# Optimization experiments

Measured on AMD Instinct MI355X. Metric: run time of the kernel, lower is better.

Reference implementation:

```python
import jax, jax.numpy as jnp
import numpy as np

D_MODEL = 768
N_LAYER = 4
VOCAB = 10000
N_MELS = 80
D_STATE = 16
D_CONV = 4
DT_RANK = 48          # ceil(768/16)
D_INNER = 1536        # expand * d_model
B_SZ, L_SEQ = 2, 1024


def rmsnorm(x, w, eps=1e-5):
    return x * jax.lax.rsqrt(jnp.mean(x * x, axis=-1, keepdims=True) + eps) * w


def causal_depthwise_conv(x, w, b):
    # x: (b, l, d_inner); w: (d_inner, 1, d_conv); torch Conv1d with padding=d_conv-1, truncated to l
    xc = jax.lax.conv_general_dilated(
        jnp.transpose(x, (0, 2, 1)), w, window_strides=(1,),
        padding=[(D_CONV - 1, 0)], dimension_numbers=('NCH', 'OIH', 'NCH'),
        feature_group_count=D_INNER)
    xc = xc + b[None, :, None]
    return jnp.transpose(xc, (0, 2, 1))


def selective_scan(u, dt, A, B, C, D):
    # u, dt: (b,l,d_in); A: (d_in,n); B,C: (b,l,n); D: (d_in,)
    dA = jnp.einsum('bld,dn->bldn', dt, A)
    dB_u = jnp.einsum('bld,bld,bln->bldn', dt, u, B)
    dA = jnp.clip(dA, -20, None)
    # shift dA by one step (exclusive cumulative decay), cumsum mode
    dA_shift = jnp.pad(dA[:, 1:], ((0, 0), (1, 0), (0, 0), (0, 0)))
    dA_cumsum = jnp.exp(jnp.cumsum(dA_shift, axis=1))
    x = jnp.cumsum(dB_u / (dA_cumsum + 1e-12), axis=1) * dA_cumsum
    y = jnp.einsum('bldn,bln->bld', x, C)
    return y + u * D


def mamba_block(x, rms_w, in_w, cw, cb, xp_w, dt_w, dt_b, A_log, Dp, out_w):
    h = rmsnorm(x, rms_w)
    xz = h @ in_w                       # (b,l,2*d_inner)
    xi, res = jnp.split(xz, 2, axis=-1)
    xi = jax.nn.silu(causal_depthwise_conv(xi, cw, cb))
    A = -jnp.exp(A_log.astype(jnp.float32))
    x_dbl = xi @ xp_w                   # (b,l,dt_rank+2n)
    delta = x_dbl[..., :DT_RANK]
    Bm = x_dbl[..., DT_RANK:DT_RANK + D_STATE]
    Cm = x_dbl[..., DT_RANK + D_STATE:]
    delta = jax.nn.softplus(delta @ dt_w + dt_b)
    y = selective_scan(xi, delta, A, Bm, Cm, Dp.astype(jnp.float32))
    y = y * jax.nn.silu(res)
    return y @ out_w + x


def setup_inputs():
    key = jax.random.key(0)
    ks = jax.random.split(key, 8)
    s = 0.02
    return {
        'input_ids': jax.random.randint(ks[0], (B_SZ, L_SEQ), 0, VOCAB),
        'embedding': jax.random.normal(ks[1], (VOCAB, D_MODEL), jnp.float32) * s,
        'rms_w': jnp.ones((N_LAYER, D_MODEL), jnp.float32),
        'in_proj_w': jax.random.normal(ks[2], (N_LAYER, D_MODEL, 2 * D_INNER), jnp.float32) * s,
        'conv_w': jax.random.normal(ks[3], (N_LAYER, D_INNER, 1, D_CONV), jnp.float32) * 0.1,
        'conv_b': jnp.zeros((N_LAYER, D_INNER), jnp.float32),
        'x_proj_w': jax.random.normal(ks[4], (N_LAYER, D_INNER, DT_RANK + 2 * D_STATE), jnp.float32) * s,
        'dt_proj_w': jax.random.normal(ks[5], (N_LAYER, DT_RANK, D_INNER), jnp.float32) * s,
        'dt_proj_b': jnp.zeros((N_LAYER, D_INNER), jnp.float32),
        'A_log': jnp.broadcast_to(jnp.log(jnp.arange(1, D_STATE + 1, dtype=jnp.float32)), (N_LAYER, D_INNER, D_STATE)) + 0.0,
        'D_param': jnp.ones((N_LAYER, D_INNER), jnp.float32),
        'out_proj_w': jax.random.normal(ks[6], (N_LAYER, D_INNER, D_MODEL), jnp.float32) * s,
        'norm_f_w': jnp.ones((D_MODEL,), jnp.float32),
        'head_w': jax.random.normal(ks[7], (D_MODEL, N_MELS), jnp.float32) * s,
    }


def reference(input_ids, embedding, rms_w, in_proj_w, conv_w, conv_b, x_proj_w,
              dt_proj_w, dt_proj_b, A_log, D_param, out_proj_w, norm_f_w, head_w):
    x = embedding[input_ids]            # (b,l,d)
    for i in range(N_LAYER):
        x = mamba_block(x, rms_w[i], in_proj_w[i], conv_w[i], conv_b[i],
                        x_proj_w[i], dt_proj_w[i], dt_proj_b[i], A_log[i],
                        D_param[i], out_proj_w[i])
    x = rmsnorm(x, norm_f_w)
    return x @ head_w                   # (b,l,n_mels)
```

## Files before the change

kernel.cpp:

```cpp
#include <hip/hip_runtime.h>
#include <hip/hip_bf16.h>
#include <math.h>

#define D_MODEL 768
#define N_LAYER 4
#define D_STATE 16
#define D_CONV  4
#define DT_RANK 48
#define D_INNER 1536
#define B_SZ    2
#define L_SEQ   1024
#define N_MELS  80
#define ROWS    (B_SZ * L_SEQ)

typedef __bf16 bf16x8 __attribute__((ext_vector_type(8)));
typedef float  f32x4  __attribute__((ext_vector_type(4)));

__device__ __forceinline__ float fast_exp2(float x) {
    float r; asm("v_exp_f32 %0, %1" : "=v"(r) : "v"(x)); return r;
}
__device__ __forceinline__ float fast_exp(float x) {
    return fast_exp2(x * 1.44269504f);
}
__device__ __forceinline__ float fast_rcp(float x) {
    float r; asm("v_rcp_f32 %0, %1" : "=v"(r) : "v"(x)); return r;
}
__device__ __forceinline__ float silu_f(float v) {
    return v * fast_rcp(1.0f + fast_exp(-v));
}
__device__ __forceinline__ float softplus_f(float v) {
    return fmaxf(v, 0.0f) + log1pf(expf(-fabsf(v)));
}
__device__ __forceinline__ unsigned short f2bf(float f) {
    unsigned int u = __float_as_uint(f);
    unsigned int r = (u + 0x7FFFu + ((u >> 16) & 1u)) >> 16;
    return (unsigned short)r;
}
__device__ __forceinline__ float bf2f(unsigned short v) {
    return __uint_as_float(((unsigned int)v) << 16);
}

__global__ void embed_kernel(const int* __restrict__ ids,
                             const float* __restrict__ emb,
                             float* __restrict__ x) {
    int i = blockIdx.x * 256 + threadIdx.x;
    if (i >= ROWS * D_MODEL) return;
    int r = i / D_MODEL, c = i - r * D_MODEL;
    x[i] = emb[(size_t)ids[r] * D_MODEL + c];
}

__global__ void rmsnorm_kernel(const float* __restrict__ x,
                               const float* __restrict__ w,
                               unsigned short* __restrict__ hb) {
    int row = blockIdx.x;
    const float* xr = x + (size_t)row * D_MODEL;
    int tid = threadIdx.x;
    float p = 0.f;
    for (int c = tid; c < D_MODEL; c += 256) { float v = xr[c]; p = fmaf(v, v, p); }
    for (int off = 32; off >= 1; off >>= 1) p += __shfl_down(p, off, 64);
    __shared__ float ws[4];
    int lane = tid & 63, wv = tid >> 6;
    if (lane == 0) ws[wv] = p;
    __syncthreads();
    if (tid == 0) ws[0] = ws[0] + ws[1] + ws[2] + ws[3];
    __syncthreads();
    float scale = 1.0f / sqrtf(ws[0] / (float)D_MODEL + 1e-5f);
    for (int c = tid; c < D_MODEL; c += 256)
        hb[(size_t)row * D_MODEL + c] = f2bf(xr[c] * scale * w[c]);
}

__global__ void prep_weights_kernel(const float* __restrict__ in_wi,
                                    const float* __restrict__ out_wi,
                                    const float* __restrict__ xp_wi,
                                    const float* __restrict__ dt_wi,
                                    unsigned short* __restrict__ wt_in,
                                    unsigned short* __restrict__ wt_out,
                                    unsigned short* __restrict__ xpT,
                                    unsigned short* __restrict__ dtwT) {
    __shared__ float t[32][33];
    int bx = blockIdx.x;
    int tid = threadIdx.x;
    if (bx < 3456) {
        const float* src; unsigned short* dst; int R, C, cy, cx;
        if (bx < 2304) {
            src = in_wi; dst = wt_in; R = D_MODEL; C = 2 * D_INNER;
            cy = bx / 96; cx = bx - cy * 96;
        } else {
            int tt = bx - 2304;
            src = out_wi; dst = wt_out; R = D_INNER; C = D_MODEL;
            cy = tt / 24; cx = tt - cy * 24;
        }
        int tx = tid & 31, ty = tid >> 5;
        int r0 = cy * 32, c0 = cx * 32;
#pragma unroll
        for (int i = 0; i < 4; i++)
            t[ty + i * 8][tx] = src[(size_t)(r0 + ty + i * 8) * C + c0 + tx];
        __syncthreads();
#pragma unroll
        for (int i = 0; i < 4; i++)
            dst[(size_t)(c0 + ty + i * 8) * R + r0 + tx] = f2bf(t[tx][ty + i * 8]);
    } else {
        int i = (bx - 3456) * 256 + tid;
        if (i < 80 * D_INNER) {
            int c = i / D_INNER, r = i - c * D_INNER;
            xpT[i] = f2bf(xp_wi[(size_t)r * 80 + c]);
        } else {
            int i2 = i - 80 * D_INNER;
            int c = i2 >> 6, r = i2 & 63;
            dtwT[i2] = (r < DT_RANK) ? f2bf(dt_wi[(size_t)r * D_INNER + c])
                                     : (unsigned short)0;
        }
    }
}

__global__ void transpose_u16_kernel(const unsigned short* __restrict__ src,
                                     unsigned short* __restrict__ dst,
                                     int R, int C) {
    __shared__ unsigned short t[32][34];
    int tx = threadIdx.x & 31, ty = threadIdx.x >> 5;
    int r0 = blockIdx.y * 32, c0 = blockIdx.x * 32;
#pragma unroll
    for (int i = 0; i < 4; i++)
        t[ty + i * 8][tx] = src[(size_t)(r0 + ty + i * 8) * C + c0 + tx];
    __syncthreads();
#pragma unroll
    for (int i = 0; i < 4; i++)
        dst[(size_t)(c0 + ty + i * 8) * R + r0 + tx] = t[tx][ty + i * 8];
}

__global__ void transpose_pad_bf16_kernel(const float* __restrict__ src,
                                          unsigned short* __restrict__ dst,
                                          int R, int C, int Rpad) {
    int i = blockIdx.x * 256 + threadIdx.x;
    if (i >= C * Rpad) return;
    int c = i / Rpad, r = i - c * Rpad;
    dst[i] = (r < R) ? f2bf(src[(size_t)r * C + c]) : (unsigned short)0;
}

__global__ void reduce_cvt_kernel(const float* __restrict__ part,
                                  float* __restrict__ xdbl,
                                  unsigned short* __restrict__ xdblb,
                                  int nsplit) {
    int i = blockIdx.x * 256 + threadIdx.x;
    if (i >= ROWS * 80) return;
    float s = 0.f;
    for (int k = 0; k < nsplit; k++) s += part[(size_t)k * ROWS * 80 + i];
    xdbl[i] = s;
    int r = i / 80, c = i - r * 80;
    if (c < DT_RANK) xdblb[r * 64 + c] = f2bf(s);
    else if (c >= 64) xdblb[r * 64 + c - 16] = 0;
}

__global__ void reduce_split_kernel(const float* __restrict__ part,
                                    float* __restrict__ dst,
                                    int MN, int nsplit) {
    int i = blockIdx.x * 256 + threadIdx.x;
    if (i >= MN) return;
    float s = 0.f;
    for (int k = 0; k < nsplit; k++) s += part[(size_t)k * MN + i];
    dst[i] = s;
}

__global__ __launch_bounds__(256) void mfma_gemm64(
        const unsigned short* __restrict__ A,
        const unsigned short* __restrict__ BT,
        const float* __restrict__ bias, const float* __restrict__ resid,
        float* __restrict__ Cf, unsigned short* __restrict__ Cb,
        int M, int N, int K, int ldc, int act, int bias_mode) {
    __shared__ unsigned short As[64][40];
    __shared__ unsigned short Bs[128][40];
    int tid = threadIdx.x;
    int row0 = blockIdx.y * 64, col0 = blockIdx.x * 128;
    int wave = tid >> 6, lane = tid & 63;
    int wr = (wave >> 1) * 32, wc = (wave & 1) * 64;
    int lm = lane & 15, lq = lane >> 4;
    int ar = tid >> 2, aseg = tid & 3;
    const unsigned short* Ap  = A  + (size_t)(row0 + ar) * K + aseg * 8;
    int br0 = tid >> 2, br1 = (tid + 256) >> 2;
    const unsigned short* Bp0 = BT + (size_t)(col0 + br0) * K + aseg * 8;
    const unsigned short* Bp1 = BT + (size_t)(col0 + br1) * K + aseg * 8;
    f32x4 acc[2][4] = {};
    bf16x8 pa  = *(const bf16x8*)Ap;
    bf16x8 pb0 = *(const bf16x8*)Bp0;
    bf16x8 pb1 = *(const bf16x8*)Bp1;
    *(bf16x8*)&As[ar][aseg * 8]  = pa;
    *(bf16x8*)&Bs[br0][aseg * 8] = pb0;
    *(bf16x8*)&Bs[br1][aseg * 8] = pb1;
    for (int k0 = 0; k0 < K; k0 += 32) {
        __syncthreads();
        bool more = (k0 + 32 < K);
        if (more) {
            pa  = *(const bf16x8*)(Ap  + k0 + 32);
            pb0 = *(const bf16x8*)(Bp0 + k0 + 32);
            pb1 = *(const bf16x8*)(Bp1 + k0 + 32);
        }
        bf16x8 af[2], bfr[4];
#pragma unroll
        for (int i = 0; i < 2; i++) af[i] = *(const bf16x8*)&As[wr + i * 16 + lm][lq * 8];
#pragma unroll
        for (int j = 0; j < 4; j++) bfr[j] = *(const bf16x8*)&Bs[wc + j * 16 + lm][lq * 8];
#pragma unroll
        for (int i = 0; i < 2; i++)
#pragma unroll
            for (int j = 0; j < 4; j++)
                acc[i][j] = __builtin_amdgcn_mfma_f32_16x16x32_bf16(af[i], bfr[j], acc[i][j], 0, 0, 0);
        __syncthreads();
        if (more) {
            *(bf16x8*)&As[ar][aseg * 8]  = pa;
            *(bf16x8*)&Bs[br0][aseg * 8] = pb0;
            *(bf16x8*)&Bs[br1][aseg * 8] = pb1;
        }
    }
#pragma unroll
    for (int i = 0; i < 2; i++) {
#pragma unroll
        for (int ii = 0; ii < 4; ii++) {
            int row = row0 + wr + i * 16 + lq * 4 + ii;
#pragma unroll
            for (int j = 0; j < 4; j++) {
                int col = col0 + wc + j * 16 + lm;
                float v = acc[i][j][ii];
                if (bias) v += bias[bias_mode ? row : col];
                if (act == 1) v = softplus_f(v);
                if (resid) v += resid[(size_t)row * ldc + col];
                if (Cf) Cf[(size_t)row * ldc + col] = v;
                else    Cb[(size_t)row * ldc + col] = f2bf(v);
            }
        }
    }
}

__global__ __launch_bounds__(256) void mfma_gemm32(
        const unsigned short* __restrict__ A,
        const unsigned short* __restrict__ BT,
        const float* __restrict__ bias, const float* __restrict__ resid,
        float* __restrict__ Cf, unsigned short* __restrict__ Cb,
        int M, int N, int K, int ldc, int act, int bias_mode) {
    __shared__ unsigned short As[32][40];
    __shared__ unsigned short Bs[128][40];
    int tid = threadIdx.x;
    int row0 = blockIdx.y * 32, col0 = blockIdx.x * 128;
    int wave = tid >> 6, lane = tid & 63;
    int wc = wave * 32;
    int lm = lane & 15, lq = lane >> 4;
    int ar = tid >> 2, aseg = tid & 3;
    const unsigned short* Ap  = A  + (size_t)(row0 + ar) * K + aseg * 8;
    int br0 = tid >> 2, br1 = (tid + 256) >> 2;
    const unsigned short* Bp0 = BT + (size_t)(col0 + br0) * K + aseg * 8;
    const unsigned short* Bp1 = BT + (size_t)(col0 + br1) * K + aseg * 8;
    bool haveA = (tid < 128);
    f32x4 acc[2][2] = {};
    bf16x8 pa = {};
    if (haveA) pa = *(const bf16x8*)Ap;
    bf16x8 pb0 = *(const bf16x8*)Bp0;
    bf16x8 pb1 = *(const bf16x8*)Bp1;
    if (haveA) *(bf16x8*)&As[ar][aseg * 8] = pa;
    *(bf16x8*)&Bs[br0][aseg * 8] = pb0;
    *(bf16x8*)&Bs[br1][aseg * 8] = pb1;
    for (int k0 = 0; k0 < K; k0 += 32) {
        __syncthreads();
        bool more = (k0 + 32 < K);
        if (more) {
            if (haveA) pa = *(const bf16x8*)(Ap + k0 + 32);
            pb0 = *(const bf16x8*)(Bp0 + k0 + 32);
            pb1 = *(const bf16x8*)(Bp1 + k0 + 32);
        }
        bf16x8 af[2], bfr[2];
#pragma unroll
        for (int i = 0; i < 2; i++) af[i] = *(const bf16x8*)&As[i * 16 + lm][lq * 8];
#pragma unroll
        for (int j = 0; j < 2; j++) bfr[j] = *(const bf16x8*)&Bs[wc + j * 16 + lm][lq * 8];
#pragma unroll
        for (int i = 0; i < 2; i++)
#pragma unroll
            for (int j = 0; j < 2; j++)
                acc[i][j] = __builtin_amdgcn_mfma_f32_16x16x32_bf16(af[i], bfr[j], acc[i][j], 0, 0, 0);
        __syncthreads();
        if (more) {
            if (haveA) *(bf16x8*)&As[ar][aseg * 8] = pa;
            *(bf16x8*)&Bs[br0][aseg * 8] = pb0;
            *(bf16x8*)&Bs[br1][aseg * 8] = pb1;
        }
    }
#pragma unroll
    for (int i = 0; i < 2; i++) {
#pragma unroll
        for (int ii = 0; ii < 4; ii++) {
            int row = row0 + i * 16 + lq * 4 + ii;
#pragma unroll
            for (int j = 0; j < 2; j++) {
                int col = col0 + wc + j * 16 + lm;
                float v = acc[i][j][ii];
                if (bias) v += bias[bias_mode ? row : col];
                if (act == 1) v = softplus_f(v);
                if (resid) v += resid[(size_t)row * ldc + col];
                if (Cf) Cf[(size_t)row * ldc + col] = v;
                else    Cb[(size_t)row * ldc + col] = f2bf(v);
            }
        }
    }
}

__global__ __launch_bounds__(256) void mfma_skinny(
        const unsigned short* __restrict__ A,
        const unsigned short* __restrict__ BT,
        float* __restrict__ part,
        int M, int K, int kchunk) {
    constexpr int N = 80, NT = 5;
    __shared__ unsigned short As[128][40];
    __shared__ unsigned short Bs[80][40];
    int tid = threadIdx.x;
    int row0 = blockIdx.x * 128;
    int kb = blockIdx.y * kchunk, ke = kb + kchunk;
    float* myout = part + (size_t)blockIdx.y * M * N;
    int wave = tid >> 6, lane = tid & 63;
    int wr = wave * 32;
    int lm = lane & 15, lq = lane >> 4;
    int ar0 = tid >> 2, ar1 = (tid + 256) >> 2, aseg = tid & 3;
    const unsigned short* Ap0 = A + (size_t)(row0 + ar0) * K + aseg * 8;
    const unsigned short* Ap1 = A + (size_t)(row0 + ar1) * K + aseg * 8;
    const unsigned short* Bp0 = BT + (size_t)ar0 * K + aseg * 8;
    const unsigned short* Bp1 = BT + (size_t)ar1 * K + aseg * 8;
    bool haveB1 = (tid < 64);
    f32x4 acc[2][NT] = {};
    bf16x8 pa0 = *(const bf16x8*)(Ap0 + kb);
    bf16x8 pa1 = *(const bf16x8*)(Ap1 + kb);
    bf16x8 pb0 = *(const bf16x8*)(Bp0 + kb);
    bf16x8 pb1 = {};
    if (haveB1) pb1 = *(const bf16x8*)(Bp1 + kb);
    *(bf16x8*)&As[ar0][aseg * 8] = pa0;
    *(bf16x8*)&As[ar1][aseg * 8] = pa1;
    *(bf16x8*)&Bs[ar0][aseg * 8] = pb0;
    if (haveB1) *(bf16x8*)&Bs[ar1][aseg * 8] = pb1;
    for (int k0 = kb; k0 < ke; k0 += 32) {
        __syncthreads();
        bool more = (k0 + 32 < ke);
        if (more) {
            pa0 = *(const bf16x8*)(Ap0 + k0 + 32);
            pa1 = *(const bf16x8*)(Ap1 + k0 + 32);
            pb0 = *(const bf16x8*)(Bp0 + k0 + 32);
            if (haveB1) pb1 = *(const bf16x8*)(Bp1 + k0 + 32);
        }
        bf16x8 af[2], bfr[NT];
#pragma unroll
        for (int i = 0; i < 2; i++) af[i] = *(const bf16x8*)&As[wr + i * 16 + lm][lq * 8];
#pragma unroll
        for (int j = 0; j < NT; j++) bfr[j] = *(const bf16x8*)&Bs[j * 16 + lm][lq * 8];
#pragma unroll
        for (int i = 0; i < 2; i++)
#pragma unroll
            for (int j = 0; j < NT; j++)
                acc[i][j] = __builtin_amdgcn_mfma_f32_16x16x32_bf16(af[i], bfr[j], acc[i][j], 0, 0, 0);
        __syncthreads();
        if (more) {
            *(bf16x8*)&As[ar0][aseg * 8] = pa0;
            *(bf16x8*)&As[ar1][aseg * 8] = pa1;
            *(bf16x8*)&Bs[ar0][aseg * 8] = pb0;
            if (haveB1) *(bf16x8*)&Bs[ar1][aseg * 8] = pb1;
        }
    }
#pragma unroll
    for (int i = 0; i < 2; i++) {
#pragma unroll
        for (int ii = 0; ii < 4; ii++) {
            int row = row0 + wr + i * 16 + lq * 4 + ii;
#pragma unroll
            for (int j = 0; j < NT; j++) {
                int col = j * 16 + lm;
                myout[(size_t)row * N + col] = acc[i][j][ii];
            }
        }
    }
}

__global__ __launch_bounds__(256) void conv_silu_kernel(
        const unsigned short* __restrict__ xzb,
        const float* __restrict__ cw,
        const float* __restrict__ cb,
        unsigned short* __restrict__ ub,
        float* __restrict__ uT,
        unsigned short* __restrict__ resT) {
    __shared__ unsigned short s_xz[67][66];
    __shared__ float us[64][65];
    int tid = threadIdx.x;
    int d0 = blockIdx.x * 64, r0 = blockIdx.y * 64;
    bool atStart = (r0 & (L_SEQ - 1)) == 0;
    for (int idx = tid; idx < 67 * 64; idx += 256) {
        int rr = idx >> 6, cc2 = idx & 63;
        unsigned short v = 0;
        if (rr >= 3 || !atStart)
            v = xzb[(size_t)(r0 - 3 + rr) * (2 * D_INNER) + d0 + cc2];
        s_xz[rr][cc2] = v;
    }
    __syncthreads();
    int cc = tid & 63, ty = tid >> 6;
    const float* wp = cw + (size_t)(d0 + cc) * D_CONV;
    float w0 = wp[0], w1 = wp[1], w2 = wp[2], w3 = wp[3];
    float bb = cb[d0 + cc];
    for (int rr = ty; rr < 64; rr += 4) {
        float s = bb;
        s = fmaf(bf2f(s_xz[rr + 0][cc]), w0, s);
        s = fmaf(bf2f(s_xz[rr + 1][cc]), w1, s);
        s = fmaf(bf2f(s_xz[rr + 2][cc]), w2, s);
        s = fmaf(bf2f(s_xz[rr + 3][cc]), w3, s);
        float v = silu_f(s);
        ub[(size_t)(r0 + rr) * D_INNER + d0 + cc] = f2bf(v);
        us[rr][cc] = v;
    }
    __syncthreads();
    int tx = tid & 63, dy = tid >> 6;
    for (int dd = dy; dd < 64; dd += 4)
        uT[(size_t)(d0 + dd) * ROWS + r0 + tx] = us[tx][dd];
    __syncthreads();
    for (int idx = tid; idx < 64 * 64; idx += 256) {
        int rr = idx >> 6, cc2 = idx & 63;
        s_xz[rr][cc2] = xzb[(size_t)(r0 + rr) * (2 * D_INNER) + D_INNER + d0 + cc2];
    }
    __syncthreads();
    for (int dd = dy; dd < 64; dd += 4)
        resT[(size_t)(d0 + dd) * ROWS + r0 + tx] = s_xz[tx][dd];
}

__global__ __launch_bounds__(256) void scan_kernel(
        const float* __restrict__ deltaT,
        const float* __restrict__ uT,
        const float* __restrict__ xdbl,
        const unsigned short* __restrict__ resT,
        const float* __restrict__ A_log,
        const float* __restrict__ Dp,
        unsigned short* __restrict__ ygT) {
    int tid = threadIdx.x;
    int n = tid & 15, c = tid >> 4;
    int bd = blockIdx.x;
    int b = bd / D_INNER, d = bd - b * D_INNER;
    int row0 = b * L_SEQ;
    float a2 = -fast_exp(A_log[d * D_STATE + n]) * 1.44269504f;
    float Dd = Dp[d];
    __shared__ float2 s_du[L_SEQ + 16];
    __shared__ float cs1[16][17];
    __shared__ float cs2[16][17];
    __shared__ float gmv[16];
    const float* dptr = deltaT + (size_t)d * ROWS + row0;
    const float* uptr = uT + (size_t)d * ROWS + row0;
    for (int e = tid; e < L_SEQ; e += 256)
        s_du[e + (e >> 6)] = make_float2(dptr[e], uptr[e]);
    __syncthreads();
    {
        int l0 = c * 64, sb = l0 + c;
        bool notfirst = (c != 0);
        float sum = 0.f;
#pragma unroll 8
        for (int j = 0; j < 64; j++) {
            float dA = fmaxf(s_du[sb + j].x * a2, -28.8539008f);
            if (j > 0 || notfirst) sum += dA;
        }
        cs1[n][c] = sum;
    }
    __syncthreads();
    float cbase = 0.f;
    for (int cc = 0; cc < c; cc++) cbase += cs1[n][cc];
    float gm = cbase;
    gm = fmaxf(gm, __shfl_xor(gm, 1, 16));
    gm = fmaxf(gm, __shfl_xor(gm, 2, 16));
    gm = fmaxf(gm, __shfl_xor(gm, 4, 16));
    gm = fmaxf(gm, __shfl_xor(gm, 8, 16));
    if (n == 0) gmv[c] = gm;
    __syncthreads();
    int lc = 16;
    for (int cc = 1; cc < 16; cc++)
        if (gmv[cc] <= -150.0f) { lc = cc; break; }
    int clen = lc * 4;
    int l0b = c * clen;
    int lend = lc * 64;
    {
        float sum = 0.f;
        for (int j = 0; j < clen; j++) {
            int l = l0b + j;
            float dA = fmaxf(s_du[l + (l >> 6)].x * a2, -28.8539008f);
            if (l > 0) sum += dA;
        }
        cs1[n][c] = sum;
    }
    __syncthreads();
    float cbase_b = 0.f;
    for (int cc = 0; cc < c; cc++) cbase_b += cs1[n][cc];
    const float* xBbase = xdbl + (size_t)row0 * 80 + DT_RANK + n;
    {
        float Cacc = cbase_b, psum = 0.f;
        for (int j = 0; j < clen; j++) {
            int l = l0b + j;
            float2 du = s_du[l + (l >> 6)];
            float dA = fmaxf(du.x * a2, -28.8539008f);
            if (l > 0) Cacc += dA;
            float S = fast_exp2(Cacc);
            float r = fast_rcp(S + 1e-12f);
            psum = fmaf(du.x * du.y * xBbase[l * 80], r, psum);
        }
        cs2[n][c] = psum;
    }
    __syncthreads();
    float pbase = 0.f;
    for (int cc = 0; cc < c; cc++) pbase += cs2[n][cc];
    {
        float Cacc = cbase_b, P = pbase;
        for (int j = 0; j < clen; j++) {
            int l = l0b + j;
            float2 du = s_du[l + (l >> 6)];
            float dA = fmaxf(du.x * a2, -28.8539008f);
            if (l > 0) Cacc += dA;
            float S = fast_exp2(Cacc);
            float r = fast_rcp(S + 1e-12f);
            P = fmaf(du.x * du.y * xBbase[l * 80], r, P);
            float contrib = P * S * xBbase[l * 80 + 16];
            contrib += __shfl_xor(contrib, 1, 16);
            contrib += __shfl_xor(contrib, 2, 16);
            contrib += __shfl_xor(contrib, 4, 16);
            contrib += __shfl_xor(contrib, 8, 16);
            if (n == 0) s_du[l + (l >> 6)].x = contrib + du.y * Dd;
        }
    }
    __syncthreads();
    const unsigned short* rptr = resT + (size_t)d * ROWS + row0;
    unsigned short* yout = ygT + (size_t)d * ROWS + row0;
    for (int e = tid; e < L_SEQ; e += 256) {
        float2 v = s_du[e + (e >> 6)];
        float y = (e < lend) ? v.x : v.y * Dd;
        float res = bf2f(rptr[e]);
        yout[e] = f2bf(y * silu_f(res));
    }
}

extern "C" void kernel_launch(void* const* d_in, const int* in_sizes, int n_in,
                              void* d_out, int out_size, void* d_ws, size_t ws_size,
                              hipStream_t stream) {
    const int*   ids    = (const int*)d_in[0];
    const float* emb    = (const float*)d_in[1];
    const float* rms_w  = (const float*)d_in[2];
    const float* in_w   = (const float*)d_in[3];
    const float* conv_w = (const float*)d_in[4];
    const float* conv_b = (const float*)d_in[5];
    const float* xp_w   = (const float*)d_in[6];
    const float* dt_w   = (const float*)d_in[7];
    const float* dt_b   = (const float*)d_in[8];
    const float* A_log  = (const float*)d_in[9];
    const float* Dp     = (const float*)d_in[10];
    const float* out_w  = (const float*)d_in[11];
    const float* nf_w   = (const float*)d_in[12];
    const float* head_w = (const float*)d_in[13];
    float* out = (float*)d_out;

    char* base = (char*)d_ws;
    float*          x      = (float*)(base + 0);
    unsigned short* hb     = (unsigned short*)(base + 6291456);
    unsigned short* xzb    = (unsigned short*)(base + 9437184);
    unsigned short* ygT    = (unsigned short*)(base + 9437184);
    unsigned short* ygb    = (unsigned short*)(base + 15728640);
    float*          uT     = (float*)(base + 22020096);
    unsigned short* ub     = (unsigned short*)(base + 34603008);
    float*          xdbl   = (float*)(base + 40894464);
    unsigned short* xdblb  = (unsigned short*)(base + 41549824);
    float*          deltaT = (float*)(base + 41811968);
    float*          part   = (float*)(base + 41811968);
    unsigned short* resT   = (unsigned short*)(base + 54394880);
    unsigned short* wt_in  = (unsigned short*)(base + 60686336);
    unsigned short* wt_out = (unsigned short*)(base + 65404928);
    unsigned short* xpT    = (unsigned short*)(base + 67764224);
    unsigned short* dtwT   = (unsigned short*)(base + 68009984);
    unsigned short* headT  = (unsigned short*)(base + 68206592);

    embed_kernel<<<(ROWS * D_MODEL + 255) / 256, 256, 0, stream>>>(ids, emb, x);
    transpose_pad_bf16_kernel<<<(N_MELS * D_MODEL + 255) / 256, 256, 0, stream>>>(
        head_w, headT, D_MODEL, N_MELS, D_MODEL);

    for (int i = 0; i < N_LAYER; i++) {
        const float* in_wi   = in_w + (size_t)i * D_MODEL * 2 * D_INNER;
        const float* conv_wi = conv_w + (size_t)i * D_INNER * D_CONV;
        const float* conv_bi = conv_b + (size_t)i * D_INNER;
        const float* xp_wi   = xp_w + (size_t)i * D_INNER * (DT_RANK + 2 * D_STATE);
        const float* dt_wi   = dt_w + (size_t)i * DT_RANK * D_INNER;
        const float* dt_bi   = dt_b + (size_t)i * D_INNER;
        const float* A_li    = A_log + (size_t)i * D_INNER * D_STATE;
        const float* Dpi     = Dp + (size_t)i * D_INNER;
        const float* out_wi  = out_w + (size_t)i * D_INNER * D_MODEL;
        const float* rms_wi  = rms_w + (size_t)i * D_MODEL;

        prep_weights_kernel<<<4320, 256, 0, stream>>>(
            in_wi, out_wi, xp_wi, dt_wi, wt_in, wt_out, xpT, dtwT);

        rmsnorm_kernel<<<ROWS, 256, 0, stream>>>(x, rms_wi, hb);
        mfma_gemm64<<<dim3(2 * D_INNER / 128, ROWS / 64), 256, 0, stream>>>(
            hb, wt_in, nullptr, nullptr, nullptr, xzb,
            ROWS, 2 * D_INNER, D_MODEL, 2 * D_INNER, 0, 0);
        conv_silu_kernel<<<dim3(D_INNER / 64, ROWS / 64), 256, 0, stream>>>(
            xzb, conv_wi, conv_bi, ub, uT, resT);
        mfma_skinny<<<dim3(ROWS / 128, 16), 256, 0, stream>>>(
            ub, xpT, part, ROWS, D_INNER, D_INNER / 16);
        reduce_cvt_kernel<<<(ROWS * 80 + 255) / 256, 256, 0, stream>>>(
            part, xdbl, xdblb, 16);
        mfma_gemm32<<<dim3(ROWS / 128, D_INNER / 32), 256, 0, stream>>>(
            dtwT, xdblb, dt_bi, nullptr, deltaT, nullptr,
            D_INNER, ROWS, 64, ROWS, 1, 1);
        scan_kernel<<<B_SZ * D_INNER, 256, 0, stream>>>(
            deltaT, uT, xdbl, resT, A_li, Dpi, ygT);
        transpose_u16_kernel<<<dim3(ROWS / 32, D_INNER / 32), 256, 0, stream>>>(
            ygT, ygb, D_INNER, ROWS);
        mfma_gemm32<<<dim3(D_MODEL / 128, ROWS / 32), 256, 0, stream>>>(
            ygb, wt_out, nullptr, x, x, nullptr,
            ROWS, D_MODEL, D_INNER, D_MODEL, 0, 0);
    }

    rmsnorm_kernel<<<ROWS, 256, 0, stream>>>(x, nf_w, hb);
    mfma_skinny<<<dim3(ROWS / 128, 8), 256, 0, stream>>>(
        hb, headT, part, ROWS, D_MODEL, D_MODEL / 8);
    reduce_split_kernel<<<(ROWS * N_MELS + 255) / 256, 256, 0, stream>>>(
        part, out, ROWS * N_MELS, 8);
}
```

Before: 710.6 us.

## Use 128x128 double-buffered GEMM with direct global-to-LDS loads for projections

Replaces the 64x128 register-staged GEMM with a 128x128-tile kernel in which each wave computes a 64x64 sub-tile. Operand tiles are loaded straight into double-buffered LDS with global_load_lds, and the next tile's load overlaps the current MFMA work. The kernel is used for both the in_proj and out_proj GEMMs, aiming for more operand reuse and less register staging. In exchange the grid gets much smaller (only 96 blocks for out_proj), which may leave CUs idle. The unpadded 32-element LDS row stride may also cause bank conflicts on fragment reads.

```diff
diff --git a/kernel.cpp b/kernel.cpp
--- a/kernel.cpp
+++ b/kernel.cpp
@@ -38,6 +38,12 @@
 }
 __device__ __forceinline__ float bf2f(unsigned short v) {
     return __uint_as_float(((unsigned int)v) << 16);
+}
+
+typedef __attribute__((address_space(1))) const unsigned int gconst_u32;
+typedef __attribute__((address_space(3))) unsigned int lds_u32;
+__device__ __forceinline__ void gload16(void* lds, const void* g) {
+    __builtin_amdgcn_global_load_lds((gconst_u32*)g, (lds_u32*)lds, 16, 0, 0);
 }
 
 __global__ void embed_kernel(const int* __restrict__ ids,
@@ -161,58 +167,59 @@
     dst[i] = s;
 }
 
-__global__ __launch_bounds__(256) void mfma_gemm64(
+__global__ __launch_bounds__(256) void mfma_gemm128(
         const unsigned short* __restrict__ A,
         const unsigned short* __restrict__ BT,
         const float* __restrict__ bias, const float* __restrict__ resid,
         float* __restrict__ Cf, unsigned short* __restrict__ Cb,
         int M, int N, int K, int ldc, int act, int bias_mode) {
-    __shared__ unsigned short As[64][40];
-    __shared__ unsigned short Bs[128][40];
+    __shared__ __align__(16) unsigned short As[2][128 * 32];
+    __shared__ __align__(16) unsigned short Bs[2][128 * 32];
     int tid = threadIdx.x;
-    int row0 = blockIdx.y * 64, col0 = blockIdx.x * 128;
+    int row0 = blockIdx.y * 128, col0 = blockIdx.x * 128;
     int wave = tid >> 6, lane = tid & 63;
-    int wr = (wave >> 1) * 32, wc = (wave & 1) * 64;
+    int wr = (wave >> 1) * 64, wc = (wave & 1) * 64;
     int lm = lane & 15, lq = lane >> 4;
-    int ar = tid >> 2, aseg = tid & 3;
-    const unsigned short* Ap  = A  + (size_t)(row0 + ar) * K + aseg * 8;
-    int br0 = tid >> 2, br1 = (tid + 256) >> 2;
-    const unsigned short* Bp0 = BT + (size_t)(col0 + br0) * K + aseg * 8;
-    const unsigned short* Bp1 = BT + (size_t)(col0 + br1) * K + aseg * 8;
-    f32x4 acc[2][4] = {};
-    bf16x8 pa  = *(const bf16x8*)Ap;
-    bf16x8 pb0 = *(const bf16x8*)Bp0;
-    bf16x8 pb1 = *(const bf16x8*)Bp1;
-    *(bf16x8*)&As[ar][aseg * 8]  = pa;
-    *(bf16x8*)&Bs[br0][aseg * 8] = pb0;
-    *(bf16x8*)&Bs[br1][aseg * 8] = pb1;
-    for (int k0 = 0; k0 < K; k0 += 32) {
-        __syncthreads();
-        bool more = (k0 + 32 < K);
-        if (more) {
-            pa  = *(const bf16x8*)(Ap  + k0 + 32);
-            pb0 = *(const bf16x8*)(Bp0 + k0 + 32);
-            pb1 = *(const bf16x8*)(Bp1 + k0 + 32);
-        }
-        bf16x8 af[2], bfr[4];
-#pragma unroll
-        for (int i = 0; i < 2; i++) af[i] = *(const bf16x8*)&As[wr + i * 16 + lm][lq * 8];
-#pragma unroll
-        for (int j = 0; j < 4; j++) bfr[j] = *(const bf16x8*)&Bs[wc + j * 16 + lm][lq * 8];
-#pragma unroll
-        for (int i = 0; i < 2; i++)
+    int srow = tid >> 2, scol = (tid & 3) * 8;
+    const unsigned short* Ap0 = A  + (size_t)(row0 + srow) * K + scol;
+    const unsigned short* Ap1 = A  + (size_t)(row0 + 64 + srow) * K + scol;
+    const unsigned short* Bp0 = BT + (size_t)(col0 + srow) * K + scol;
+    const unsigned short* Bp1 = BT + (size_t)(col0 + 64 + srow) * K + scol;
+    int wbase = wave * 512;
+    f32x4 acc[4][4] = {};
+    gload16(&As[0][wbase], Ap0);
+    gload16(&As[0][2048 + wbase], Ap1);
+    gload16(&Bs[0][wbase], Bp0);
+    gload16(&Bs[0][2048 + wbase], Bp1);
+    __syncthreads();
+    int nk = K >> 5;
+    int cur = 0;
+    for (int t = 0; t < nk; ++t) {
+        int cn = cur ^ 1;
+        if (t + 1 < nk) {
+            int ko = (t + 1) << 5;
+            gload16(&As[cn][wbase], Ap0 + ko);
+            gload16(&As[cn][2048 + wbase], Ap1 + ko);
+            gload16(&Bs[cn][wbase], Bp0 + ko);
+            gload16(&Bs[cn][2048 + wbase], Bp1 + ko);
+        }
+        bf16x8 af[4], bfr[4];
+#pragma unroll
+        for (int i = 0; i < 4; i++)
+            af[i] = *(const bf16x8*)&As[cur][(wr + i * 16 + lm) * 32 + lq * 8];
+#pragma unroll
+        for (int j = 0; j < 4; j++)
+            bfr[j] = *(const bf16x8*)&Bs[cur][(wc + j * 16 + lm) * 32 + lq * 8];
+#pragma unroll
+        for (int i = 0; i < 4; i++)
 #pragma unroll
             for (int j = 0; j < 4; j++)
                 acc[i][j] = __builtin_amdgcn_mfma_f32_16x16x32_bf16(af[i], bfr[j], acc[i][j], 0, 0, 0);
         __syncthreads();
-        if (more) {
-            *(bf16x8*)&As[ar][aseg * 8]  = pa;
-            *(bf16x8*)&Bs[br0][aseg * 8] = pb0;
-            *(bf16x8*)&Bs[br1][aseg * 8] = pb1;
-        }
-    }
-#pragma unroll
-    for (int i = 0; i < 2; i++) {
+        cur = cn;
+    }
+#pragma unroll
+    for (int i = 0; i < 4; i++) {
 #pragma unroll
         for (int ii = 0; ii < 4; ii++) {
             int row = row0 + wr + i * 16 + lq * 4 + ii;
@@ -588,7 +595,7 @@
             in_wi, out_wi, xp_wi, dt_wi, wt_in, wt_out, xpT, dtwT);
 
         rmsnorm_kernel<<<ROWS, 256, 0, stream>>>(x, rms_wi, hb);
-        mfma_gemm64<<<dim3(2 * D_INNER / 128, ROWS / 64), 256, 0, stream>>>(
+        mfma_gemm128<<<dim3(2 * D_INNER / 128, ROWS / 128), 256, 0, stream>>>(
             hb, wt_in, nullptr, nullptr, nullptr, xzb,
             ROWS, 2 * D_INNER, D_MODEL, 2 * D_INNER, 0, 0);
         conv_silu_kernel<<<dim3(D_INNER / 64, ROWS / 64), 256, 0, stream>>>(
@@ -604,7 +611,7 @@
             deltaT, uT, xdbl, resT, A_li, Dpi, ygT);
         transpose_u16_kernel<<<dim3(ROWS / 32, D_INNER / 32), 256, 0, stream>>>(
             ygT, ygb, D_INNER, ROWS);
-        mfma_gemm32<<<dim3(D_MODEL / 128, ROWS / 32), 256, 0, stream>>>(
+        mfma_gemm128<<<dim3(D_MODEL / 128, ROWS / 128), 256, 0, stream>>>(
             ygb, wt_out, nullptr, x, x, nullptr,
             ROWS, D_MODEL, D_INNER, D_MODEL, 0, 0);
     }
```

New measurement: 834.9 us. 1.17x slower.

## Use direct global-to-LDS loads with double-buffered 64-wide K tiles in MFMA GEMMs

Applied to the files above, without the earlier changes.

Both MFMA GEMM kernels now load tiles straight into LDS with global_load_lds, bypassing registers. They double-buffer the shared tiles so the next K-tile loads while the current one computes. The K step grows from 32 to 64, which halves the number of barriers per iteration. The unpadded 64-element row layout may cause LDS bank conflicts, and the kernels now require K to be a multiple of 64.

```diff
diff --git a/kernel.cpp b/kernel.cpp
--- a/kernel.cpp
+++ b/kernel.cpp
@@ -38,6 +38,12 @@
 }
 __device__ __forceinline__ float bf2f(unsigned short v) {
     return __uint_as_float(((unsigned int)v) << 16);
+}
+
+typedef __attribute__((address_space(1))) const unsigned int gconst_u32;
+typedef __attribute__((address_space(3))) unsigned int lds_u32;
+__device__ __forceinline__ void gload16(void* lds, const void* g) {
+    __builtin_amdgcn_global_load_lds((gconst_u32*)g, (lds_u32*)lds, 16, 0, 0);
 }
 
 __global__ void embed_kernel(const int* __restrict__ ids,
@@ -167,49 +173,58 @@
         const float* __restrict__ bias, const float* __restrict__ resid,
         float* __restrict__ Cf, unsigned short* __restrict__ Cb,
         int M, int N, int K, int ldc, int act, int bias_mode) {
-    __shared__ unsigned short As[64][40];
-    __shared__ unsigned short Bs[128][40];
+    __shared__ __align__(16) unsigned short As[2][64 * 64];
+    __shared__ __align__(16) unsigned short Bs[2][128 * 64];
     int tid = threadIdx.x;
     int row0 = blockIdx.y * 64, col0 = blockIdx.x * 128;
     int wave = tid >> 6, lane = tid & 63;
     int wr = (wave >> 1) * 32, wc = (wave & 1) * 64;
     int lm = lane & 15, lq = lane >> 4;
-    int ar = tid >> 2, aseg = tid & 3;
-    const unsigned short* Ap  = A  + (size_t)(row0 + ar) * K + aseg * 8;
-    int br0 = tid >> 2, br1 = (tid + 256) >> 2;
-    const unsigned short* Bp0 = BT + (size_t)(col0 + br0) * K + aseg * 8;
-    const unsigned short* Bp1 = BT + (size_t)(col0 + br1) * K + aseg * 8;
+    int srow = tid >> 3, seg = tid & 7;
+    const unsigned short* ApA = A  + (size_t)(row0 + srow) * K + seg * 8;
+    const unsigned short* ApB = A  + (size_t)(row0 + 32 + srow) * K + seg * 8;
+    const unsigned short* Bp0 = BT + (size_t)(col0 + srow) * K + seg * 8;
+    const unsigned short* Bp1 = BT + (size_t)(col0 + 32 + srow) * K + seg * 8;
+    const unsigned short* Bp2 = BT + (size_t)(col0 + 64 + srow) * K + seg * 8;
+    const unsigned short* Bp3 = BT + (size_t)(col0 + 96 + srow) * K + seg * 8;
+    int wb = wave * 512;
     f32x4 acc[2][4] = {};
-    bf16x8 pa  = *(const bf16x8*)Ap;
-    bf16x8 pb0 = *(const bf16x8*)Bp0;
-    bf16x8 pb1 = *(const bf16x8*)Bp1;
-    *(bf16x8*)&As[ar][aseg * 8]  = pa;
-    *(bf16x8*)&Bs[br0][aseg * 8] = pb0;
-    *(bf16x8*)&Bs[br1][aseg * 8] = pb1;
-    for (int k0 = 0; k0 < K; k0 += 32) {
+    gload16(&As[0][wb], ApA);
+    gload16(&As[0][2048 + wb], ApB);
+    gload16(&Bs[0][wb], Bp0);
+    gload16(&Bs[0][2048 + wb], Bp1);
+    gload16(&Bs[0][4096 + wb], Bp2);
+    gload16(&Bs[0][6144 + wb], Bp3);
+    __syncthreads();
+    int nk = K >> 6, cur = 0;
+    for (int t = 0; t < nk; ++t) {
+        int cn = cur ^ 1;
+        if (t + 1 < nk) {
+            int ko = (t + 1) << 6;
+            gload16(&As[cn][wb], ApA + ko);
+            gload16(&As[cn][2048 + wb], ApB + ko);
+            gload16(&Bs[cn][wb], Bp0 + ko);
+            gload16(&Bs[cn][2048 + wb], Bp1 + ko);
+            gload16(&Bs[cn][4096 + wb], Bp2 + ko);
+            gload16(&Bs[cn][6144 + wb], Bp3 + ko);
+        }
+#pragma unroll
+        for (int ks = 0; ks < 2; ks++) {
+            bf16x8 af[2], bfr[4];
+#pragma unroll
+            for (int i = 0; i < 2; i++)
+                af[i] = *(const bf16x8*)&As[cur][(wr + i * 16 + lm) * 64 + ks * 32 + lq * 8];
+#pragma unroll
+            for (int j = 0; j < 4; j++)
+                bfr[j] = *(const bf16x8*)&Bs[cur][(wc + j * 16 + lm) * 64 + ks * 32 + lq * 8];
+#pragma unroll
+            for (int i = 0; i < 2; i++)
+#pragma unroll
+                for (int j = 0; j < 4; j++)
+                    acc[i][j] = __builtin_amdgcn_mfma_f32_16x16x32_bf16(af[i], bfr[j], acc[i][j], 0, 0, 0);
+        }
         __syncthreads();
-        bool more = (k0 + 32 < K);
-        if (more) {
-            pa  = *(const bf16x8*)(Ap  + k0 + 32);
-            pb0 = *(const bf16x8*)(Bp0 + k0 + 32);
-            pb1 = *(const bf16x8*)(Bp1 + k0 + 32);
-        }
-        bf16x8 af[2], bfr[4];
-#pragma unroll
-        for (int i = 0; i < 2; i++) af[i] = *(const bf16x8*)&As[wr + i * 16 + lm][lq * 8];
-#pragma unroll
-        for (int j = 0; j < 4; j++) bfr[j] = *(const bf16x8*)&Bs[wc + j * 16 + lm][lq * 8];
-#pragma unroll
-        for (int i = 0; i < 2; i++)
-#pragma unroll
-            for (int j = 0; j < 4; j++)
-                acc[i][j] = __builtin_amdgcn_mfma_f32_16x16x32_bf16(af[i], bfr[j], acc[i][j], 0, 0, 0);
-        __syncthreads();
-        if (more) {
-            *(bf16x8*)&As[ar][aseg * 8]  = pa;
-            *(bf16x8*)&Bs[br0][aseg * 8] = pb0;
-            *(bf16x8*)&Bs[br1][aseg * 8] = pb1;
-        }
+        cur = cn;
     }
 #pragma unroll
     for (int i = 0; i < 2; i++) {
@@ -236,51 +251,55 @@
         const float* __restrict__ bias, const float* __restrict__ resid,
         float* __restrict__ Cf, unsigned short* __restrict__ Cb,
         int M, int N, int K, int ldc, int act, int bias_mode) {
-    __shared__ unsigned short As[32][40];
-    __shared__ unsigned short Bs[128][40];
+    __shared__ __align__(16) unsigned short As[2][32 * 64];
+    __shared__ __align__(16) unsigned short Bs[2][128 * 64];
     int tid = threadIdx.x;
     int row0 = blockIdx.y * 32, col0 = blockIdx.x * 128;
     int wave = tid >> 6, lane = tid & 63;
     int wc = wave * 32;
     int lm = lane & 15, lq = lane >> 4;
-    int ar = tid >> 2, aseg = tid & 3;
-    const unsigned short* Ap  = A  + (size_t)(row0 + ar) * K + aseg * 8;
-    int br0 = tid >> 2, br1 = (tid + 256) >> 2;
-    const unsigned short* Bp0 = BT + (size_t)(col0 + br0) * K + aseg * 8;
-    const unsigned short* Bp1 = BT + (size_t)(col0 + br1) * K + aseg * 8;
-    bool haveA = (tid < 128);
+    int srow = tid >> 3, seg = tid & 7;
+    const unsigned short* ApA = A  + (size_t)(row0 + srow) * K + seg * 8;
+    const unsigned short* Bp0 = BT + (size_t)(col0 + srow) * K + seg * 8;
+    const unsigned short* Bp1 = BT + (size_t)(col0 + 32 + srow) * K + seg * 8;
+    const unsigned short* Bp2 = BT + (size_t)(col0 + 64 + srow) * K + seg * 8;
+    const unsigned short* Bp3 = BT + (size_t)(col0 + 96 + srow) * K + seg * 8;
+    int wb = wave * 512;
     f32x4 acc[2][2] = {};
-    bf16x8 pa = {};
-    if (haveA) pa = *(const bf16x8*)Ap;
-    bf16x8 pb0 = *(const bf16x8*)Bp0;
-    bf16x8 pb1 = *(const bf16x8*)Bp1;
-    if (haveA) *(bf16x8*)&As[ar][aseg * 8] = pa;
-    *(bf16x8*)&Bs[br0][aseg * 8] = pb0;
-    *(bf16x8*)&Bs[br1][aseg * 8] = pb1;
-    for (int k0 = 0; k0 < K; k0 += 32) {
+    gload16(&As[0][wb], ApA);
+    gload16(&Bs[0][wb], Bp0);
+    gload16(&Bs[0][2048 + wb], Bp1);
+    gload16(&Bs[0][4096 + wb], Bp2);
+    gload16(&Bs[0][6144 + wb], Bp3);
+    __syncthreads();
+    int nk = K >> 6, cur = 0;
+    for (int t = 0; t < nk; ++t) {
+        int cn = cur ^ 1;
+        if (t + 1 < nk) {
+            int ko = (t + 1) << 6;
+            gload16(&As[cn][wb], ApA + ko);
+            gload16(&Bs[cn][wb], Bp0 + ko);
+            gload16(&Bs[cn][2048 + wb], Bp1 + ko);
+            gload16(&Bs[cn][4096 + wb], Bp2 + ko);
+            gload16(&Bs[cn][6144 + wb], Bp3 + ko);
+        }
+#pragma unroll
+        for (int ks = 0; ks < 2; ks++) {
+            bf16x8 af[2], bfr[2];
+#pragma unroll
+            for (int i = 0; i < 2; i++)
+                af[i] = *(const bf16x8*)&As[cur][(i * 16 + lm) * 64 + ks * 32 + lq * 8];
+#pragma unroll
+            for (int j = 0; j < 2; j++)
+                bfr[j] = *(const bf16x8*)&Bs[cur][(wc + j * 16 + lm) * 64 + ks * 32 + lq * 8];
+#pragma unroll
+            for (int i = 0; i < 2; i++)
+#pragma unroll
+                for (int j = 0; j < 2; j++)
+                    acc[i][j] = __builtin_amdgcn_mfma_f32_16x16x32_bf16(af[i], bfr[j], acc[i][j], 0, 0, 0);
+        }
         __syncthreads();
-        bool more = (k0 + 32 < K);
-        if (more) {
-            if (haveA) pa = *(const bf16x8*)(Ap + k0 + 32);
-            pb0 = *(const bf16x8*)(Bp0 + k0 + 32);
-            pb1 = *(const bf16x8*)(Bp1 + k0 + 32);
-        }
-        bf16x8 af[2], bfr[2];
-#pragma unroll
-        for (int i = 0; i < 2; i++) af[i] = *(const bf16x8*)&As[i * 16 + lm][lq * 8];
-#pragma unroll
-        for (int j = 0; j < 2; j++) bfr[j] = *(const bf16x8*)&Bs[wc + j * 16 + lm][lq * 8];
-#pragma unroll
-        for (int i = 0; i < 2; i++)
-#pragma unroll
-            for (int j = 0; j < 2; j++)
-                acc[i][j] = __builtin_amdgcn_mfma_f32_16x16x32_bf16(af[i], bfr[j], acc[i][j], 0, 0, 0);
-        __syncthreads();
-        if (more) {
-            if (haveA) *(bf16x8*)&As[ar][aseg * 8] = pa;
-            *(bf16x8*)&Bs[br0][aseg * 8] = pb0;
-            *(bf16x8*)&Bs[br1][aseg * 8] = pb1;
-        }
+        cur = cn;
     }
 #pragma unroll
     for (int i = 0; i < 2; i++) {
```

New measurement: 703.3 us. About the same (-1.0%).
